# Kernel tuning notes

Measured on AMD Instinct MI355X. Metric: run time of the kernel, lower is better.

## Reference

```python
import jax, jax.numpy as jnp
import numpy as np
from jax import lax

WS = 7          # window size
SHIFT = 3       # shift size
HEADS = 16
DIM = 512
NREF = 100
H_IMG = 112
W_IMG = 112
BATCH = 2
HD = DIM // HEADS
SCALE = HD ** (-0.5)
EPS = 1e-5


def _layernorm(x, w, b):
    mu = jnp.mean(x, axis=-1, keepdims=True)
    var = jnp.mean((x - mu) ** 2, axis=-1, keepdims=True)
    return (x - mu) / jnp.sqrt(var + EPS) * w + b


def _rel_pos_index():
    coords = np.stack(np.meshgrid(np.arange(WS), np.arange(WS), indexing='ij'))  # (2,ws,ws)
    cf = coords.reshape(2, -1)
    rel = cf[:, :, None] - cf[:, None, :]
    rel = rel.transpose(1, 2, 0).astype(np.int64)
    rel[..., 0] += WS - 1
    rel[..., 1] += WS - 1
    rel[..., 0] *= 2 * WS - 1
    return rel.sum(-1).reshape(-1)  # (N*N,)

_RPI = _rel_pos_index()


def setup_inputs() -> dict:
    key = jax.random.key(0)
    ks = jax.random.split(key, 16)
    C = DIM
    s = 0.02
    x = jax.random.normal(ks[0], (BATCH, H_IMG * W_IMG, C), jnp.float32)
    x_ref = jax.random.normal(ks[1], (BATCH, NREF, C), jnp.float32)
    # shifted-window attention mask (standard Swin construction)
    img = np.zeros((H_IMG, W_IMG))
    cnt = 0
    for hs in (slice(0, -WS), slice(-WS, -SHIFT), slice(-SHIFT, None)):
        for ws_ in (slice(0, -WS), slice(-WS, -SHIFT), slice(-SHIFT, None)):
            img[hs, ws_] = cnt
            cnt += 1
    mw = img.reshape(H_IMG // WS, WS, W_IMG // WS, WS).transpose(0, 2, 1, 3).reshape(-1, WS * WS)
    am = mw[:, None, :] - mw[:, :, None]
    mask = jnp.asarray(np.where(am != 0, -100.0, 0.0), jnp.float32)  # (nW, N, N)
    return dict(
        x=x, x_ref=x_ref, mask=mask,
        norm1_w=jnp.ones((C,), jnp.float32), norm1_b=jnp.zeros((C,), jnp.float32),
        qkv_w=jax.random.normal(ks[2], (3 * C, C), jnp.float32) * s,
        qkv_b=jnp.zeros((3 * C,), jnp.float32),
        diff_mu=jax.random.normal(ks[3], (1, 1, C), jnp.float32),
        diff_logsigma=jax.random.normal(ks[4], (1, 1, C), jnp.float32) * s,
        rpb_table=jax.random.normal(ks[5], ((2 * WS - 1) ** 2, HEADS), jnp.float32) * s,
        ref_qk_w=jax.random.normal(ks[6], (2 * C, C), jnp.float32) * s,
        ref_qk_b=jnp.zeros((2 * C,), jnp.float32),
        conv_w=jax.random.normal(ks[7], (HEADS, HEADS, 3, 3), jnp.float32) * s,
        conv_b=jnp.zeros((HEADS,), jnp.float32),
        proj_w=jax.random.normal(ks[8], (C, C), jnp.float32) * s,
        proj_b=jnp.zeros((C,), jnp.float32),
        norm2_w=jnp.ones((C,), jnp.float32), norm2_b=jnp.zeros((C,), jnp.float32),
        fc1_w=jax.random.normal(ks[9], (4 * C, C), jnp.float32) * s,
        fc1_b=jnp.zeros((4 * C,), jnp.float32),
        fc2_w=jax.random.normal(ks[10], (C, 4 * C), jnp.float32) * s,
        fc2_b=jnp.zeros((C,), jnp.float32),
        Hh=H_IMG, Ww=W_IMG,
    )


def _window_attention(xw, mask, x_ref, qkv_w, qkv_b, diff_mu, diff_logsigma,
                      rpb_table, ref_qk_w, ref_qk_b, conv_w, conv_b, proj_w, proj_b):
    B_, N, C = xw.shape
    rB = x_ref.shape[0]
    n_win = B_ // rB
    qkv = (xw @ qkv_w.T + qkv_b).reshape(B_, N, 3, HEADS, HD).transpose(2, 0, 3, 1, 4)
    q, k, v = qkv[0], qkv[1], qkv[2]  # (B_, heads, N, hd)
    # reference tokens -> q/v with reparameterized shift/scale
    ref_qk = (x_ref @ ref_qk_w.T + ref_qk_b).reshape(rB, NREF, 2, C).transpose(2, 0, 1, 3)
    ref_q = diff_mu + jnp.exp(diff_logsigma) * ref_qk[0]
    ref_q = ref_q.reshape(rB, NREF, HEADS, HD).transpose(0, 2, 1, 3)
    ref_v = ref_qk[1].reshape(rB, NREF, HEADS, HD).transpose(0, 2, 1, 3)
    ref_k = jnp.repeat(ref_q, n_win, axis=0)  # (B_, heads, nref, hd)
    ref_v = jnp.repeat(ref_v, n_win, axis=0)
    ra = jnp.einsum('bhnd,bhrd->bhnr', q, ref_k)  # (B_, heads, N, nref)
    ra = ra.reshape(rB, n_win, HEADS, N, NREF).transpose(0, 2, 1, 3, 4).reshape(rB, HEADS, n_win * N, NREF)
    # 3 rounds of conv diffusion + layernorm(no affine) + gelu, residual
    for _ in range(3):
        u = lax.conv_general_dilated(ra, conv_w, (1, 1), 'SAME',
                                     dimension_numbers=('NCHW', 'OIHW', 'NCHW'))
        u = u + conv_b[None, :, None, None]
        mu = jnp.mean(u, axis=(-2, -1), keepdims=True)
        var = jnp.mean((u - mu) ** 2, axis=(-2, -1), keepdims=True)
        u = jax.nn.gelu((u - mu) / jnp.sqrt(var + EPS), approximate=False)
        ra = ra + u
    ra = ra.reshape(rB, HEADS, n_win, N, NREF).transpose(0, 2, 1, 3, 4).reshape(B_, HEADS, N, NREF)
    ra = jax.nn.softmax(ra, axis=-1)
    q_new = jnp.einsum('bhnr,bhrd->bhnd', ra, ref_v) * SCALE
    attn = jnp.einsum('bhnd,bhmd->bhnm', q_new, k)
    rpb = rpb_table[_RPI].reshape(N, N, HEADS).transpose(2, 0, 1)  # (heads, N, N)
    attn = attn + rpb[None]
    nW = mask.shape[0]
    attn = attn.reshape(B_ // nW, nW, HEADS, N, N) + mask[None, :, None]
    attn = jax.nn.softmax(attn.reshape(B_, HEADS, N, N), axis=-1)
    out = jnp.einsum('bhnm,bhmd->bhnd', attn, v).transpose(0, 2, 1, 3).reshape(B_, N, C)
    return out @ proj_w.T + proj_b


def reference(x, x_ref, mask, norm1_w, norm1_b, qkv_w, qkv_b, diff_mu, diff_logsigma,
              rpb_table, ref_qk_w, ref_qk_b, conv_w, conv_b, proj_w, proj_b,
              norm2_w, norm2_b, fc1_w, fc1_b, fc2_w, fc2_b, Hh, Ww):
    B, L, C = x.shape
    shortcut = x
    xn = _layernorm(x, norm1_w, norm1_b).reshape(B, Hh, Ww, C)
    # cyclic shift
    sx = jnp.roll(xn, (-SHIFT, -SHIFT), axis=(1, 2))
    # window partition -> (B*nWin, ws*ws, C)
    xw = sx.reshape(B, Hh // WS, WS, Ww // WS, WS, C).transpose(0, 1, 3, 2, 4, 5).reshape(-1, WS * WS, C)
    aw = _window_attention(xw, mask, x_ref, qkv_w, qkv_b, diff_mu, diff_logsigma,
                           rpb_table, ref_qk_w, ref_qk_b, conv_w, conv_b, proj_w, proj_b)
    # window reverse
    sx = aw.reshape(B, Hh // WS, Ww // WS, WS, WS, C).transpose(0, 1, 3, 2, 4, 5).reshape(B, Hh, Ww, C)
    xn = jnp.roll(sx, (SHIFT, SHIFT), axis=(1, 2)).reshape(B, L, C)
    x = shortcut + xn
    h = _layernorm(x, norm2_w, norm2_b)
    h = jax.nn.gelu(h @ fc1_w.T + fc1_b, approximate=False)
    return x + (h @ fc2_w.T + fc2_b)
```

## Files before the change

### kernel.cpp

```cpp
#include <hip/hip_runtime.h>
#include <hip/hip_bf16.h>

typedef __attribute__((ext_vector_type(8))) short short8;
typedef __attribute__((ext_vector_type(8))) unsigned short ushort8;
typedef __attribute__((ext_vector_type(4))) float f32x4;
typedef __attribute__((ext_vector_type(4))) unsigned int u32x4;
typedef __attribute__((ext_vector_type(2))) unsigned int u32x2;

#define DEV __device__ __forceinline__

DEV float gelu_f(float x) { return 0.5f * x * (1.f + erff(x * 0.70710678118654752440f)); }

DEV float bf2f(unsigned short s) {
  unsigned int t = ((unsigned int)s) << 16;
  float f; __builtin_memcpy(&f, &t, 4); return f;
}
DEV unsigned short f2bf(float f) {
  __hip_bfloat16 b = __float2bfloat16(f);
  unsigned short s; __builtin_memcpy(&s, &b, 2); return s;
}

DEV void async_copy16(void* lds, const void* g) {
  __builtin_amdgcn_global_load_lds(
      (const __attribute__((address_space(1))) unsigned int*)g,
      (__attribute__((address_space(3))) unsigned int*)lds, 16, 0, 0);
}

DEV void block_reduce2(float& s, float& s2) {
  __shared__ float red[8];
  int tid = threadIdx.x;
#pragma unroll
  for (int o = 32; o > 0; o >>= 1) { s += __shfl_down(s, o); s2 += __shfl_down(s2, o); }
  if ((tid & 63) == 0) { red[tid >> 6] = s; red[4 + (tid >> 6)] = s2; }
  __syncthreads();
  s  = red[0] + red[1] + red[2] + red[3];
  s2 = red[4] + red[5] + red[6] + red[7];
}

__global__ __launch_bounds__(256) void f2b_all_kernel(
    const float* __restrict__ qkv_w, const float* __restrict__ proj_w,
    const float* __restrict__ fc1_w, const float* __restrict__ fc2_w,
    __hip_bfloat16* __restrict__ wq, __hip_bfloat16* __restrict__ wp,
    __hip_bfloat16* __restrict__ w1, __hip_bfloat16* __restrict__ w2) {
  int i = blockIdx.x * 256 + threadIdx.x;
  const float* src; unsigned short* dst; int o;
  if (i < 98304)       { src = qkv_w;  dst = (unsigned short*)wq; o = i; }
  else if (i < 131072) { src = proj_w; dst = (unsigned short*)wp; o = i - 98304; }
  else if (i < 262144) { src = fc1_w;  dst = (unsigned short*)w1; o = i - 131072; }
  else                 { src = fc2_w;  dst = (unsigned short*)w2; o = i - 262144; }
  f32x4 a = *reinterpret_cast<const f32x4*>(&src[(size_t)o * 8]);
  f32x4 b = *reinterpret_cast<const f32x4*>(&src[(size_t)o * 8 + 4]);
  ushort8 v;
#pragma unroll
  for (int j = 0; j < 4; j++) { v[j] = f2bf(a[j]); v[4 + j] = f2bf(b[j]); }
  *reinterpret_cast<ushort8*>(&dst[(size_t)o * 8]) = v;
}

__global__ __launch_bounds__(256) void maskb_kernel(const float* __restrict__ mask,
                                                    unsigned short* __restrict__ maskB) {
  int i = blockIdx.x * 256 + threadIdx.x;
  int m = i % 56, rest = i / 56;
  int n = rest % 49, win = rest / 49;
  unsigned short v = 0;
  if (m < 49) v = f2bf(mask[((size_t)win * 49 + n) * 49 + m]);
  maskB[i] = v;
}

__global__ __launch_bounds__(256) void rpbt_kernel(const float* __restrict__ rpb,
                                                   unsigned short* __restrict__ rpbT) {
  int i = blockIdx.x * 256 + threadIdx.x;
  if (i >= 43904) return;
  int m = i % 56, rest = i / 56;
  int n = rest % 49, h = rest / 49;
  unsigned short v = 0;
  if (m < 49) {
    int rp = (n / 7 - m / 7 + 6) * 13 + (n % 7 - m % 7 + 6);
    v = f2bf(rpb[rp * 16 + h]);
  }
  rpbT[i] = v;
}

__global__ __launch_bounds__(256) void cwt_kernel(const float* __restrict__ cw,
                                                  unsigned short* __restrict__ cwT) {
  int i = blockIdx.x * 256 + threadIdx.x;
  if (i >= 2560) return;
  int co = i / 160, k = i % 160;
  unsigned short v = 0;
  if (k < 144) {
    int ci = k & 15, p = k >> 4;
    v = f2bf(cw[(co * 16 + ci) * 9 + p]);
  }
  cwT[i] = v;
}

__global__ __launch_bounds__(256) void ln1_window_kernel(
    const float* __restrict__ x, const float* __restrict__ w, const float* __restrict__ b,
    __hip_bfloat16* __restrict__ xw) {
  int tid = threadIdx.x;
  int wave = tid >> 6, lane = tid & 63;
  int t = blockIdx.x * 4 + wave;
  int b_ = t / 49, n = t % 49;
  int bb = b_ >> 8, win = b_ & 255;
  int wi = win >> 4, wj = win & 15;
  int ii = n / 7, jj = n % 7;
  int sh = (wi * 7 + ii + 3) % 112;
  int sw = (wj * 7 + jj + 3) % 112;
  const float* row = x + ((size_t)bb * 12544 + sh * 112 + sw) * 512;
  f32x4 v0 = *reinterpret_cast<const f32x4*>(&row[lane * 8]);
  f32x4 v1 = *reinterpret_cast<const f32x4*>(&row[lane * 8 + 4]);
  float s = 0.f, s2 = 0.f;
#pragma unroll
  for (int j = 0; j < 4; j++) {
    s += v0[j] + v1[j];
    s2 += v0[j] * v0[j] + v1[j] * v1[j];
  }
#pragma unroll
  for (int o = 1; o < 64; o <<= 1) { s += __shfl_xor(s, o); s2 += __shfl_xor(s2, o); }
  float mu = s * (1.f / 512.f);
  float rstd = rsqrtf(s2 * (1.f / 512.f) - mu * mu + 1e-5f);
  f32x4 w0 = *reinterpret_cast<const f32x4*>(&w[lane * 8]);
  f32x4 w1 = *reinterpret_cast<const f32x4*>(&w[lane * 8 + 4]);
  f32x4 c0 = *reinterpret_cast<const f32x4*>(&b[lane * 8]);
  f32x4 c1 = *reinterpret_cast<const f32x4*>(&b[lane * 8 + 4]);
  ushort8 o8;
#pragma unroll
  for (int j = 0; j < 4; j++) {
    o8[j]     = f2bf((v0[j] - mu) * rstd * w0[j] + c0[j]);
    o8[4 + j] = f2bf((v1[j] - mu) * rstd * w1[j] + c1[j]);
  }
  *reinterpret_cast<ushort8*>((unsigned short*)xw + (size_t)t * 512 + lane * 8) = o8;
}

template <int EPI>
__global__ __launch_bounds__(256) void gemm_bt(
    const __hip_bfloat16* __restrict__ A, const __hip_bfloat16* __restrict__ B,
    const float* __restrict__ bias, float* __restrict__ outF,
    __hip_bfloat16* __restrict__ outB, int M, int N, int K) {
  __shared__ __align__(16) __hip_bfloat16 As[2][128 * 64];
  __shared__ __align__(16) __hip_bfloat16 Bs[2][128 * 64];
  int nn = N >> 7;
  int nblk = gridDim.x;
  int bid = blockIdx.x;
  int xcd = bid & 7, slot = bid >> 3;
  int q8 = nblk >> 3, r8 = nblk & 7;
  int base = xcd < r8 ? xcd * (q8 + 1) : r8 * (q8 + 1) + (xcd - r8) * q8;
  int lin = base + slot;
  int m0 = (lin / nn) << 7, n0 = (lin % nn) << 7;
  int tid = threadIdx.x;
  int wave = tid >> 6, lane = tid & 63;
  int wm = (wave & 1) * 64, wn = (wave >> 1) * 64;
  int lrow = lane & 15, kq = lane >> 4;
  int srow = lane >> 3, scol = (lane & 7) * 8;
  int rb = wave * 32;
  const __hip_bfloat16* Abase = A + (size_t)m0 * K;
  const __hip_bfloat16* Bbase = B + (size_t)n0 * K;
#pragma unroll
  for (int i = 0; i < 4; i++) {
    int row = rb + i * 8 + srow;
    async_copy16(&As[0][(rb + i * 8) * 64], &Abase[(size_t)row * K + scol]);
    async_copy16(&Bs[0][(rb + i * 8) * 64], &Bbase[(size_t)row * K + scol]);
  }
  __syncthreads();
  f32x4 acc[4][4] = {};
  int nk = K >> 6;
  for (int t = 0; t < nk; t++) {
    int cur = t & 1;
    if (t + 1 < nk) {
      int k0 = (t + 1) << 6;
#pragma unroll
      for (int i = 0; i < 4; i++) {
        int row = rb + i * 8 + srow;
        async_copy16(&As[cur ^ 1][(rb + i * 8) * 64], &Abase[(size_t)row * K + k0 + scol]);
        async_copy16(&Bs[cur ^ 1][(rb + i * 8) * 64], &Bbase[(size_t)row * K + k0 + scol]);
      }
    }
#pragma unroll
    for (int ks = 0; ks < 2; ks++) {
      short8 af[4], bf[4];
#pragma unroll
      for (int u = 0; u < 4; u++) {
        af[u] = *reinterpret_cast<const short8*>(&As[cur][(wm + u * 16 + lrow) * 64 + ks * 32 + kq * 8]);
        bf[u] = *reinterpret_cast<const short8*>(&Bs[cur][(wn + u * 16 + lrow) * 64 + ks * 32 + kq * 8]);
      }
#pragma unroll
      for (int tm = 0; tm < 4; tm++)
#pragma unroll
        for (int tn = 0; tn < 4; tn++)
          acc[tm][tn] = __builtin_amdgcn_mfma_f32_16x16x32_bf16(af[tm], bf[tn], acc[tm][tn], 0, 0, 0);
    }
    __syncthreads();
  }
#pragma unroll
  for (int tm = 0; tm < 4; tm++) {
#pragma unroll
    for (int tn = 0; tn < 4; tn++) {
      int col = n0 + wn + tn * 16 + lrow;
      float bv = bias[col];
#pragma unroll
      for (int r = 0; r < 4; r++) {
        int row = m0 + wm + tm * 16 + kq * 4 + r;
        float v = acc[tm][tn][r] + bv;
        if (EPI == 4) {
          if (col < 512)
            ((unsigned short*)outB)[(size_t)row * 512 + col] = f2bf(v);
          else
            ((unsigned short*)outF)[(size_t)row * 1024 + (col - 512)] = f2bf(v);
        } else {
          size_t o = (size_t)row * N + col;
          if (EPI == 1) outB[o] = __float2bfloat16(v);
          else if (EPI == 2) outB[o] = __float2bfloat16(gelu_f(v));
          else outF[o] += v;
        }
      }
    }
  }
}

__global__ __launch_bounds__(256) void ref_kernel(
    const float* __restrict__ x_ref, const float* __restrict__ w, const float* __restrict__ bias,
    const float* __restrict__ diff_mu, const float* __restrict__ diff_ls,
    unsigned short* __restrict__ refq, unsigned short* __restrict__ refvT) {
  int blk = blockIdx.x;
  int b = blk / 100, r = blk % 100;
  __shared__ float xs[512];
  int tid = threadIdx.x;
  const float* xr = x_ref + (size_t)(b * 100 + r) * 512;
  xs[tid] = xr[tid];
  xs[tid + 256] = xr[tid + 256];
  __syncthreads();
#pragma unroll
  for (int cc = 0; cc < 4; cc++) {
    int c = cc * 256 + tid;
    const float* wr = w + (size_t)c * 512;
    float s = bias[c];
    for (int k = 0; k < 512; k++) s += xs[k] * wr[k];
    if (c < 512) {
      float v = diff_mu[c] + expf(diff_ls[c]) * s;
      int hh = c >> 5, d = c & 31;
      refq[((size_t)(b * 16 + hh) * 100 + r) * 32 + d] = f2bf(v);
    } else {
      int c2 = c - 512, hh = c2 >> 5, d = c2 & 31;
      refvT[(((size_t)b * 16 + hh) * 32 + d) * 128 + r] = f2bf(s);
    }
  }
  if (r < 28) {
#pragma unroll
    for (int j = 0; j < 2; j++) {
      int idx = j * 256 + tid;
      int hh = idx >> 5, d = idx & 31;
      refvT[(((size_t)b * 16 + hh) * 32 + d) * 128 + 100 + r] = 0;
    }
  }
}

__global__ __launch_bounds__(256) void ra_kernel(
    const __hip_bfloat16* __restrict__ q, const unsigned short* __restrict__ refq,
    __hip_bfloat16* __restrict__ ra) {
  __shared__ __align__(16) unsigned short q_s[64 * 40];
  __shared__ __align__(16) unsigned short rq_s[112 * 40];
  int bid = blockIdx.x;
  int blk = (bid & 7) * 1024 + (bid >> 3);
  int b_ = blk >> 4, h = blk & 15;
  int rb = b_ >> 8, win = b_ & 255;
  int tid = threadIdx.x;
  int wave = tid >> 6, lane = tid & 63;
  int lrow = lane & 15, kq = lane >> 4;
  u32x4 z4 = {};
  const unsigned short* qb = (const unsigned short*)q + (size_t)b_ * 49 * 512 + h * 32;
  for (int i = tid; i < 196; i += 256) {
    int n = i >> 2, c = i & 3;
    *reinterpret_cast<u32x4*>(&q_s[n * 40 + c * 8]) =
        *reinterpret_cast<const u32x4*>(&qb[n * 512 + c * 8]);
  }
  for (int i = tid; i < 60; i += 256) {
    int n = 49 + (i >> 2), c = i & 3;
    *reinterpret_cast<u32x4*>(&q_s[n * 40 + c * 8]) = z4;
  }
  const unsigned short* rqg = refq + (size_t)(rb * 16 + h) * 3200;
  for (int i = tid; i < 400; i += 256) {
    int r = i >> 2, c = i & 3;
    *reinterpret_cast<u32x4*>(&rq_s[r * 40 + c * 8]) =
        *reinterpret_cast<const u32x4*>(&rqg[r * 32 + c * 8]);
  }
  for (int i = tid; i < 48; i += 256) {
    int r = 100 + (i >> 2), c = i & 3;
    *reinterpret_cast<u32x4*>(&rq_s[r * 40 + c * 8]) = z4;
  }
  __syncthreads();
  short8 a = *reinterpret_cast<const short8*>(&q_s[(wave * 16 + lrow) * 40 + kq * 8]);
  unsigned short* ra_base = (unsigned short*)ra + ((size_t)(rb * 16 + h) * 12544 + win * 49) * 100;
  f32x4 zero = {};
#pragma unroll
  for (int nt = 0; nt < 7; nt++) {
    short8 b = *reinterpret_cast<const short8*>(&rq_s[(nt * 16 + lrow) * 40 + kq * 8]);
    f32x4 c = __builtin_amdgcn_mfma_f32_16x16x32_bf16(a, b, zero, 0, 0, 0);
    int col = nt * 16 + lrow;
#pragma unroll
    for (int r = 0; r < 4; r++) {
      int n = wave * 16 + kq * 4 + r;
      if (n < 49 && col < 100) ra_base[n * 100 + col] = f2bf(c[r]);
    }
  }
}

DEV int swzi(int pl, int ci) {
  int byte = (pl << 5) + (ci << 1);
  byte ^= ((pl >> 2) & 3) << 4;
  return byte >> 1;
}
__global__ __launch_bounds__(256, 6) void conv_kernel(
    const __hip_bfloat16* __restrict__ ra_, const unsigned short* __restrict__ cwT,
    const float* __restrict__ cb,
    __hip_bfloat16* __restrict__ u_, float* __restrict__ psum, float* __restrict__ psumsq) {
  __shared__ __align__(16) unsigned short in_s[6 * 103 * 16];
  __shared__ __align__(16) unsigned short st_s[4 * 16 * 36];
  __shared__ float sred_s[4][16], sred_s2[4][16];
  const unsigned short* ra = (const unsigned short*)ra_;
  unsigned short* u = (unsigned short*)u_;
  int ytb = blockIdx.x;
  int yt = (ytb & 7) * 392 + (ytb >> 3);
  int bb = blockIdx.y;
  int y0 = yt * 4;
  int tid = threadIdx.x;
  int wave = tid >> 6, lane = tid & 63;
  int lrow = lane & 15, kq = lane >> 4;
  for (int i = tid; i < 288; i += 256) {
    int ci = i & 15, rem = i >> 4;
    int yl = rem / 3, xs = rem % 3;
    int xl = (xs == 0) ? 0 : (100 + xs);
    in_s[swzi(yl * 103 + xl, ci)] = 0;
  }
  if (tid < 192) {
    int unit = tid >> 1, par = tid & 1;
    int ci = unit / 6, yl = unit % 6;
    int gy = y0 - 1 + yl;
    bool rv = (gy >= 0 && gy < 12544);
    const unsigned short* rp = ra + (((size_t)bb * 16 + ci) * 12544 + (rv ? gy : 0)) * 100;
    int plb = yl * 103 + 1;
#pragma unroll 4
    for (int c = par; c < 25; c += 2) {
      u32x2 d = {0u, 0u};
      if (rv) d = *reinterpret_cast<const u32x2*>(&rp[c * 4]);
      int pl = plb + c * 4;
      in_s[swzi(pl + 0, ci)] = (unsigned short)(d[0] & 0xffff);
      in_s[swzi(pl + 1, ci)] = (unsigned short)(d[0] >> 16);
      in_s[swzi(pl + 2, ci)] = (unsigned short)(d[1] & 0xffff);
      in_s[swzi(pl + 3, ci)] = (unsigned short)(d[1] >> 16);
    }
  }
  __syncthreads();

  short8 afr[5];
#pragma unroll
  for (int c = 0; c < 5; c++)
    afr[c] = *reinterpret_cast<const short8*>(&cwT[lrow * 160 + c * 32 + kq * 8]);
  int kqh = kq >> 1, ci0 = (kq & 1) * 8;
  int kyA[5], kxA[5];
#pragma unroll
  for (int c = 0; c < 5; c++) {
    int p = c * 2 + kqh; if (p > 8) p = 0;
    kyA[c] = p / 3; kxA[c] = p % 3;
  }
  float bias_r[4];
#pragma unroll
  for (int r = 0; r < 4; r++) bias_r[r] = cb[kq * 4 + r];
  float s_r[4] = {0.f, 0.f, 0.f, 0.f}, s2_r[4] = {0.f, 0.f, 0.f, 0.f};

  int yl = wave;
  int gy = y0 + yl;
  unsigned short* stw = &st_s[wave * 16 * 36];
  int seg = lane >> 2, part = lane & 3;
  const size_t ubase = ((size_t)bb * 16 * 12544 + gy) * 100;
#pragma unroll
  for (int xp = 0; xp < 4; xp++) {
#pragma unroll
    for (int xh = 0; xh < 2; xh++) {
      int xg = xp * 2 + xh;
      if (xg >= 7) break;
      int px = xg * 16 + lrow;
      int pxc = px < 100 ? px : 99;
      f32x4 acc = {};
#pragma unroll
      for (int c = 0; c < 5; c++) {
        short8 bfrag = *reinterpret_cast<const short8*>(
            &in_s[swzi((yl + kyA[c]) * 103 + pxc + kxA[c], ci0)]);
        acc = __builtin_amdgcn_mfma_f32_16x16x32_bf16(afr[c], bfrag, acc, 0, 0, 0);
      }
      bool valid = px < 100;
#pragma unroll
      for (int r = 0; r < 4; r++) {
        float v = acc[r] + bias_r[r];
        if (valid) {
          stw[(kq * 4 + r) * 36 + xh * 16 + lrow] = f2bf(v);
          s_r[r] += v; s2_r[r] += v * v;
        }
      }
    }
    unsigned short* ug = u + ubase + (size_t)seg * 1254400;
    if (xp < 3) {
      u32x2 d0 = *reinterpret_cast<const u32x2*>(&stw[seg * 36 + part * 4]);
      u32x2 d1 = *reinterpret_cast<const u32x2*>(&stw[seg * 36 + 16 + part * 4]);
      *reinterpret_cast<u32x2*>(&ug[xp * 32 + part * 4]) = d0;
      *reinterpret_cast<u32x2*>(&ug[xp * 32 + 16 + part * 4]) = d1;
    } else if (lane < 16) {
      u32x2 d = *reinterpret_cast<const u32x2*>(&st_s[wave * 16 * 36 + lane * 36]);
      *reinterpret_cast<u32x2*>(&u[ubase + (size_t)lane * 1254400 + 96]) = d;
    }
  }
#pragma unroll
  for (int o = 1; o < 16; o <<= 1)
#pragma unroll
    for (int r = 0; r < 4; r++) { s_r[r] += __shfl_xor(s_r[r], o); s2_r[r] += __shfl_xor(s2_r[r], o); }
  if (lrow == 0)
#pragma unroll
    for (int r = 0; r < 4; r++) { sred_s[wave][kq * 4 + r] = s_r[r]; sred_s2[wave][kq * 4 + r] = s2_r[r]; }
  __syncthreads();
  if (tid < 16) {
    float s  = sred_s[0][tid] + sred_s[1][tid] + sred_s[2][tid] + sred_s[3][tid];
    float s2 = sred_s2[0][tid] + sred_s2[1][tid] + sred_s2[2][tid] + sred_s2[3][tid];
    size_t pi = ((size_t)bb * 3136 + yt) * 16 + tid;
    psum[pi] = s; psumsq[pi] = s2;
  }
}

__global__ __launch_bounds__(256) void conv_stats_kernel(
    const float* __restrict__ psum, const float* __restrict__ psumsq, float* __restrict__ stats) {
  int g = blockIdx.x;
  int bb = g >> 4, co = g & 15;
  int tid = threadIdx.x;
  float s = 0.f, s2 = 0.f;
  for (int t = tid; t < 3136; t += 256) {
    size_t pi = ((size_t)bb * 3136 + t) * 16 + co;
    s += psum[pi];
    s2 += psumsq[pi];
  }
  block_reduce2(s, s2);
  if (tid == 0) {
    const float inv = 1.f / 1254400.f;
    float mu = s * inv;
    float var = s2 * inv - mu * mu;
    stats[g * 2] = mu;
    stats[g * 2 + 1] = rsqrtf(var + 1e-5f);
  }
}

__global__ __launch_bounds__(256) void conv_apply_kernel(
    __hip_bfloat16* __restrict__ ra, const __hip_bfloat16* __restrict__ u,
    const float* __restrict__ stats) {
  const int total8 = 5017600;
  int stride = gridDim.x * 256;
  for (int i = blockIdx.x * 256 + threadIdx.x; i < total8; i += stride) {
    int g = i / 156800;
    float mu = stats[g * 2], rstd = stats[g * 2 + 1];
    ushort8 uu = reinterpret_cast<const ushort8*>(u)[i];
    ushort8 rr = reinterpret_cast<const ushort8*>(ra)[i];
    ushort8 oo;
#pragma unroll
    for (int j = 0; j < 8; j++) {
      float rv = bf2f(rr[j]) + gelu_f((bf2f(uu[j]) - mu) * rstd);
      oo[j] = f2bf(rv);
    }
    reinterpret_cast<ushort8*>(ra)[i] = oo;
  }
}

template <int FUSE>
__global__ __launch_bounds__(256, 8) void attn_kernel(
    const __hip_bfloat16* __restrict__ ra_, const __hip_bfloat16* __restrict__ u_,
    const float* __restrict__ stats, const unsigned short* __restrict__ refvT,
    const __hip_bfloat16* __restrict__ kv_, const unsigned short* __restrict__ rpbT,
    const unsigned short* __restrict__ maskB, __hip_bfloat16* __restrict__ att_) {
  __shared__ __align__(16) char smem[18944];
  unsigned short* P1 = (unsigned short*)smem;
  unsigned short* P2 = (unsigned short*)smem;
  unsigned short* vT = (unsigned short*)(smem + 9216);
  unsigned short* qn = (unsigned short*)(smem + 13824);

#define LSUM(n) (*reinterpret_cast<float*>(&qn[(n) * 40 + 32]))

  int bid = blockIdx.x;
  int blk = (bid & 7) * 1024 + (bid >> 3);
  int b_ = blk >> 4, h = blk & 15;
  int rb = b_ >> 8, win = b_ & 255;
  int tid = threadIdx.x;
  int wave = tid >> 6, lane = tid & 63;
  int lrow = lane & 15, kq = lane >> 4;
  const unsigned short* ra = (const unsigned short*)ra_;
  const unsigned short* ug = (const unsigned short*)u_;
  const unsigned short* kv = (const unsigned short*)kv_;
  unsigned short* att = (unsigned short*)att_;
  u32x2 zz = {};

  if (tid < 64) LSUM(tid) = 1.0f;
  float mu = 0.f, rstd = 0.f;
  if (FUSE) { mu = stats[(rb * 16 + h) * 2]; rstd = stats[(rb * 16 + h) * 2 + 1]; }

  const size_t tile_off = ((size_t)(rb * 16 + h) * 12544 + win * 49) * 100;
  const unsigned short* rab = ra + tile_off;
  const unsigned short* uab = ug + tile_off;
  for (int i = tid; i < 1225; i += 256) {
    int n = i / 25, c = i % 25;
    u32x2 rv = *reinterpret_cast<const u32x2*>(&rab[n * 100 + c * 4]);
    if (FUSE) {
      u32x2 uv = *reinterpret_cast<const u32x2*>(&uab[n * 100 + c * 4]);
      unsigned short rr4[4] = {(unsigned short)(rv[0] & 0xffff), (unsigned short)(rv[0] >> 16),
                               (unsigned short)(rv[1] & 0xffff), (unsigned short)(rv[1] >> 16)};
      unsigned short uu4[4] = {(unsigned short)(uv[0] & 0xffff), (unsigned short)(uv[0] >> 16),
                               (unsigned short)(uv[1] & 0xffff), (unsigned short)(uv[1] >> 16)};
      unsigned short o4[4];
#pragma unroll
      for (int j = 0; j < 4; j++)
        o4[j] = f2bf(bf2f(rr4[j]) + gelu_f((bf2f(uu4[j]) - mu) * rstd));
      u32x2 w;
      w[0] = (unsigned int)o4[0] | ((unsigned int)o4[1] << 16);
      w[1] = (unsigned int)o4[2] | ((unsigned int)o4[3] << 16);
      *reinterpret_cast<u32x2*>(&P1[n * 136 + c * 4]) = w;
    } else {
      *reinterpret_cast<u32x2*>(&P1[n * 136 + c * 4]) = rv;
    }
  }
  for (int i = tid; i < 343; i += 256) {
    int n = i / 7, c = i % 7;
    *reinterpret_cast<u32x2*>(&P1[n * 136 + 100 + c * 4]) = zz;
  }
  __syncthreads();

  if (tid < 196) {
    int n = tid >> 2, q = tid & 3;
    unsigned short* row = P1 + n * 136 + q * 25;
    float e[25];
#pragma unroll
    for (int r = 0; r < 25; r++) e[r] = bf2f(row[r]);
    float mx = -1e30f;
#pragma unroll
    for (int r = 0; r < 25; r++) mx = fmaxf(mx, e[r]);
    mx = fmaxf(mx, __shfl_xor(mx, 1));
    mx = fmaxf(mx, __shfl_xor(mx, 2));
    float sm = 0.f;
#pragma unroll
    for (int r = 0; r < 25; r++) { e[r] = __expf(e[r] - mx); sm += e[r]; }
    sm += __shfl_xor(sm, 1);
    sm += __shfl_xor(sm, 2);
#pragma unroll
    for (int r = 0; r < 25; r++) row[r] = f2bf(e[r]);
    if (q == 0) LSUM(n) = sm;
  }
  __syncthreads();

  const unsigned short* rvtg = refvT + (size_t)(rb * 16 + h) * 4096;
  f32x4 acc1[2] = {};
#pragma unroll
  for (int ks = 0; ks < 4; ks++) {
    short8 a = *reinterpret_cast<const short8*>(&P1[(wave * 16 + lrow) * 136 + ks * 32 + kq * 8]);
#pragma unroll
    for (int dt = 0; dt < 2; dt++) {
      short8 b = *reinterpret_cast<const short8*>(&rvtg[(dt * 16 + lrow) * 128 + ks * 32 + kq * 8]);
      acc1[dt] = __builtin_amdgcn_mfma_f32_16x16x32_bf16(a, b, acc1[dt], 0, 0, 0);
    }
  }
  float invl[4];
#pragma unroll
  for (int r = 0; r < 4; r++)
    invl[r] = 0.17677669529663688f / LSUM(wave * 16 + kq * 4 + r);
#pragma unroll
  for (int dt = 0; dt < 2; dt++)
#pragma unroll
    for (int r = 0; r < 4; r++) {
      int n = wave * 16 + kq * 4 + r;
      qn[n * 40 + dt * 16 + lrow] = f2bf(acc1[dt][r] * invl[r]);
    }
  __syncthreads();

  const unsigned short* kvb = kv + (size_t)b_ * 49 * 1024;
  for (int i = tid; i < 196; i += 256) {
    int m = i >> 2, dg = (i & 3) * 8;
    ushort8 vv = *reinterpret_cast<const ushort8*>(&kvb[m * 1024 + 512 + h * 32 + dg]);
#pragma unroll
    for (int j = 0; j < 8; j++) vT[(dg + j) * 72 + m] = vv[j];
  }
  for (int i = tid; i < 480; i += 256) vT[(i / 15) * 72 + 49 + i % 15] = 0;
  __syncthreads();

  const unsigned short* bt = maskB + (size_t)win * 2744;
  const unsigned short* rt = rpbT + (size_t)h * 2744;
  short8 aq = *reinterpret_cast<const short8*>(&qn[(wave * 16 + lrow) * 40 + kq * 8]);
  f32x4 zero = {};
  float val[4][4];
#pragma unroll
  for (int mt = 0; mt < 4; mt++) {
    int mrow = mt * 16 + lrow;
    int mc = mrow < 49 ? mrow : 48;
    short8 bk = *reinterpret_cast<const short8*>(&kvb[mc * 1024 + h * 32 + kq * 8]);
    f32x4 lg = __builtin_amdgcn_mfma_f32_16x16x32_bf16(aq, bk, zero, 0, 0, 0);
    int m = mrow;
#pragma unroll
    for (int r = 0; r < 4; r++) {
      int n = wave * 16 + kq * 4 + r;
      float v;
      if (m < 49 && n < 49)
        v = lg[r] + bf2f(rt[n * 56 + m]) + bf2f(bt[n * 56 + m]);
      else v = -1e30f;
      val[mt][r] = v;
    }
  }
#pragma unroll
  for (int r = 0; r < 4; r++) {
    float mx = -1e30f;
#pragma unroll
    for (int mt = 0; mt < 4; mt++) mx = fmaxf(mx, val[mt][r]);
    mx = fmaxf(mx, __shfl_xor(mx, 1)); mx = fmaxf(mx, __shfl_xor(mx, 2));
    mx = fmaxf(mx, __shfl_xor(mx, 4)); mx = fmaxf(mx, __shfl_xor(mx, 8));
    float sm = 0.f, e[4];
#pragma unroll
    for (int mt = 0; mt < 4; mt++) { e[mt] = __expf(val[mt][r] - mx); sm += e[mt]; }
    sm += __shfl_xor(sm, 1); sm += __shfl_xor(sm, 2);
    sm += __shfl_xor(sm, 4); sm += __shfl_xor(sm, 8);
    float inv = 1.f / sm;
    int n = wave * 16 + kq * 4 + r;
#pragma unroll
    for (int mt = 0; mt < 4; mt++) P2[n * 72 + mt * 16 + lrow] = f2bf(e[mt] * inv);
  }
  __syncthreads();

  f32x4 acc2[2] = {};
#pragma unroll
  for (int ks = 0; ks < 2; ks++) {
    short8 ap = *reinterpret_cast<const short8*>(&P2[(wave * 16 + lrow) * 72 + ks * 32 + kq * 8]);
#pragma unroll
    for (int dt = 0; dt < 2; dt++) {
      short8 bv = *reinterpret_cast<const short8*>(&vT[(dt * 16 + lrow) * 72 + ks * 32 + kq * 8]);
      acc2[dt] = __builtin_amdgcn_mfma_f32_16x16x32_bf16(ap, bv, acc2[dt], 0, 0, 0);
    }
  }
  unsigned short* ab = att + (size_t)b_ * 49 * 512 + h * 32;
#pragma unroll
  for (int dt = 0; dt < 2; dt++)
#pragma unroll
    for (int r = 0; r < 4; r++) {
      int n = wave * 16 + kq * 4 + r;
      if (n < 49) ab[n * 512 + dt * 16 + lrow] = f2bf(acc2[dt][r]);
    }
#undef LSUM
}

__global__ __launch_bounds__(256) void resid_ln2_kernel(
    const float* __restrict__ x, const __hip_bfloat16* __restrict__ proj_out,
    const float* __restrict__ w2, const float* __restrict__ b2,
    float* __restrict__ out, __hip_bfloat16* __restrict__ hout) {
  int tid = threadIdx.x;
  int wave = tid >> 6, lane = tid & 63;
  int blk = blockIdx.x * 4 + wave;
  int bb = blk / 12544, l = blk % 12544;
  int hh = l / 112, ww = l % 112;
  int hs = (hh + 109) % 112, wsx = (ww + 109) % 112;
  int t = (bb * 256 + (hs / 7) * 16 + (wsx / 7)) * 49 + (hs % 7) * 7 + (wsx % 7);
  const float* xr = x + (size_t)blk * 512 + lane * 8;
  const unsigned short* pr = (const unsigned short*)proj_out + (size_t)t * 512 + lane * 8;
  f32x4 x0 = *reinterpret_cast<const f32x4*>(xr);
  f32x4 x1 = *reinterpret_cast<const f32x4*>(xr + 4);
  ushort8 p8 = *reinterpret_cast<const ushort8*>(pr);
  float v[8];
#pragma unroll
  for (int j = 0; j < 4; j++) {
    v[j]     = x0[j] + bf2f(p8[j]);
    v[4 + j] = x1[j] + bf2f(p8[4 + j]);
  }
  float s = 0.f, s2 = 0.f;
#pragma unroll
  for (int j = 0; j < 8; j++) { s += v[j]; s2 += v[j] * v[j]; }
  float* orow = out + (size_t)blk * 512 + lane * 8;
  f32x4 o0, o1;
#pragma unroll
  for (int j = 0; j < 4; j++) { o0[j] = v[j]; o1[j] = v[4 + j]; }
  *reinterpret_cast<f32x4*>(orow) = o0;
  *reinterpret_cast<f32x4*>(orow + 4) = o1;
#pragma unroll
  for (int o = 1; o < 64; o <<= 1) { s += __shfl_xor(s, o); s2 += __shfl_xor(s2, o); }
  float mu = s * (1.f / 512.f);
  float rstd = rsqrtf(s2 * (1.f / 512.f) - mu * mu + 1e-5f);
  f32x4 w0 = *reinterpret_cast<const f32x4*>(&w2[lane * 8]);
  f32x4 w1 = *reinterpret_cast<const f32x4*>(&w2[lane * 8 + 4]);
  f32x4 c0 = *reinterpret_cast<const f32x4*>(&b2[lane * 8]);
  f32x4 c1 = *reinterpret_cast<const f32x4*>(&b2[lane * 8 + 4]);
  ushort8 h8;
#pragma unroll
  for (int j = 0; j < 4; j++) {
    h8[j]     = f2bf((v[j] - mu) * rstd * w0[j] + c0[j]);
    h8[4 + j] = f2bf((v[4 + j] - mu) * rstd * w1[j] + c1[j]);
  }
  *reinterpret_cast<ushort8*>((unsigned short*)hout + (size_t)blk * 512 + lane * 8) = h8;
}

extern "C" void kernel_launch(void* const* d_in, const int* in_sizes, int n_in,
                              void* d_out, int out_size, void* d_ws, size_t ws_size,
                              hipStream_t stream) {
  const float* x       = (const float*)d_in[0];
  const float* x_ref   = (const float*)d_in[1];
  const float* mask    = (const float*)d_in[2];
  const float* n1w     = (const float*)d_in[3];
  const float* n1b     = (const float*)d_in[4];
  const float* qkv_w   = (const float*)d_in[5];
  const float* qkv_b   = (const float*)d_in[6];
  const float* diff_mu = (const float*)d_in[7];
  const float* diff_ls = (const float*)d_in[8];
  const float* rpb     = (const float*)d_in[9];
  const float* ref_w   = (const float*)d_in[10];
  const float* ref_b   = (const float*)d_in[11];
  const float* conv_w  = (const float*)d_in[12];
  const float* conv_b  = (const float*)d_in[13];
  const float* proj_w  = (const float*)d_in[14];
  const float* proj_b  = (const float*)d_in[15];
  const float* n2w     = (const float*)d_in[16];
  const float* n2b     = (const float*)d_in[17];
  const float* fc1_w   = (const float*)d_in[18];
  const float* fc1_b   = (const float*)d_in[19];
  const float* fc2_w   = (const float*)d_in[20];
  const float* fc2_b   = (const float*)d_in[21];
  float* out = (float*)d_out;

  char* ws = (char*)d_ws;
  size_t off = 0;
  auto alloc = [&](size_t bytes) -> char* {
    char* p = ws + off;
    off += (bytes + 255) & ~(size_t)255;
    return p;
  };
  __hip_bfloat16* wq_bf = (__hip_bfloat16*)alloc(1536ULL * 512 * 2);
  __hip_bfloat16* wp_bf = (__hip_bfloat16*)alloc(512ULL * 512 * 2);
  __hip_bfloat16* w1_bf = (__hip_bfloat16*)alloc(2048ULL * 512 * 2);
  __hip_bfloat16* w2_bf = (__hip_bfloat16*)alloc(512ULL * 2048 * 2);
  unsigned short* refq  = (unsigned short*)alloc(2ULL * 16 * 100 * 32 * 2);
  unsigned short* refvT = (unsigned short*)alloc(2ULL * 16 * 32 * 128 * 2);
  unsigned short* maskB = (unsigned short*)alloc(256ULL * 49 * 56 * 2);
  unsigned short* rpbT  = (unsigned short*)alloc(16ULL * 49 * 56 * 2);
  unsigned short* cwT   = (unsigned short*)alloc(2560ULL * 2);
  float* psum  = (float*)alloc(2ULL * 3136 * 16 * 4);
  float* psumq = (float*)alloc(2ULL * 3136 * 16 * 4);
  float* stats = (float*)alloc(64 * 4);
  char* regX  = alloc(25088ULL * 512 * 2);
  char* regQ  = alloc(25088ULL * 512 * 2);
  char* regRA = alloc(2ULL * 16 * 12544 * 100 * 2);
  char* regU  = alloc(2ULL * 16 * 12544 * 100 * 2);

  __hip_bfloat16* xw_bf   = (__hip_bfloat16*)regX;
  __hip_bfloat16* att_bf  = (__hip_bfloat16*)regX;
  __hip_bfloat16* q_bf    = (__hip_bfloat16*)regQ;
  __hip_bfloat16* h_bf    = (__hip_bfloat16*)regQ;
  __hip_bfloat16* ra      = (__hip_bfloat16*)regRA;
  __hip_bfloat16* hg      = (__hip_bfloat16*)regRA;
  __hip_bfloat16* u       = (__hip_bfloat16*)regU;
  __hip_bfloat16* proj_bf = (__hip_bfloat16*)(regU + 51380224);

  const size_t kv_bytes = 25088ULL * 1024 * 2;
  bool fused = (ws_size >= off + kv_bytes);
  __hip_bfloat16* kv_bf = fused ? (__hip_bfloat16*)alloc(kv_bytes)
                                : (__hip_bfloat16*)regU;

  f2b_all_kernel<<<1536, 256, 0, stream>>>(qkv_w, proj_w, fc1_w, fc2_w,
                                           wq_bf, wp_bf, w1_bf, w2_bf);
  maskb_kernel<<<2744, 256, 0, stream>>>(mask, maskB);
  rpbt_kernel<<<172, 256, 0, stream>>>(rpb, rpbT);
  cwt_kernel<<<10, 256, 0, stream>>>(conv_w, cwT);
  ln1_window_kernel<<<6272, 256, 0, stream>>>(x, n1w, n1b, xw_bf);
  if (fused) {
    gemm_bt<4><<<2352, 256, 0, stream>>>(xw_bf, wq_bf, qkv_b, (float*)kv_bf, q_bf,
                                         25088, 1536, 512);
  } else {
    gemm_bt<1><<<784, 256, 0, stream>>>(xw_bf, wq_bf, qkv_b, nullptr, q_bf,
                                        25088, 512, 512);
  }
  ref_kernel<<<200, 256, 0, stream>>>(x_ref, ref_w, ref_b, diff_mu, diff_ls, refq, refvT);
  ra_kernel<<<8192, 256, 0, stream>>>(q_bf, refq, ra);
  for (int rd = 0; rd < 3; rd++) {
    conv_kernel<<<dim3(3136, 2), 256, 0, stream>>>(ra, cwT, conv_b, u, psum, psumq);
    conv_stats_kernel<<<32, 256, 0, stream>>>(psum, psumq, stats);
    if (rd < 2 || !fused)
      conv_apply_kernel<<<4096, 256, 0, stream>>>(ra, u, stats);
  }
  if (!fused)
    gemm_bt<1><<<1568, 256, 0, stream>>>(xw_bf, wq_bf + 512 * 512, qkv_b + 512,
                                         nullptr, kv_bf, 25088, 1024, 512);
  if (fused)
    attn_kernel<1><<<8192, 256, 0, stream>>>(ra, u, stats, refvT, kv_bf, rpbT, maskB, att_bf);
  else
    attn_kernel<0><<<8192, 256, 0, stream>>>(ra, u, stats, refvT, kv_bf, rpbT, maskB, att_bf);
  gemm_bt<1><<<784, 256, 0, stream>>>(att_bf, wp_bf, proj_b, nullptr, proj_bf,
                                      25088, 512, 512);
  resid_ln2_kernel<<<6272, 256, 0, stream>>>(x, proj_bf, n2w, n2b, out, h_bf);
  for (int ch = 0; ch < 2; ch++) {
    const __hip_bfloat16* hA = h_bf + (size_t)ch * 12544 * 512;
    gemm_bt<2><<<1568, 256, 0, stream>>>(hA, w1_bf, fc1_b, nullptr, hg,
                                         12544, 2048, 512);
    gemm_bt<3><<<392, 256, 0, stream>>>(hg, w2_bf, fc2_b,
                                        out + (size_t)ch * 12544 * 512, nullptr,
                                        12544, 512, 2048);
  }
}
```

Before: 1.087 ms.

## Shrink GEMM tile to 64x128 single-buffered LDS for higher occupancy

Result: faster. 1.008 ms (-7.2%).

```diff
diff --git a/kernel.cpp b/kernel.cpp
--- a/kernel.cpp
+++ b/kernel.cpp
@@ -132,12 +132,12 @@
 }
 
 template <int EPI>
-__global__ __launch_bounds__(256) void gemm_bt(
+__global__ __launch_bounds__(256, 6) void gemm_bt(
     const __hip_bfloat16* __restrict__ A, const __hip_bfloat16* __restrict__ B,
     const float* __restrict__ bias, float* __restrict__ outF,
     __hip_bfloat16* __restrict__ outB, int M, int N, int K) {
-  __shared__ __align__(16) __hip_bfloat16 As[2][128 * 64];
-  __shared__ __align__(16) __hip_bfloat16 Bs[2][128 * 64];
+  __shared__ __align__(16) __hip_bfloat16 As[64 * 64];
+  __shared__ __align__(16) __hip_bfloat16 Bs[128 * 64];
   int nn = N >> 7;
   int nblk = gridDim.x;
   int bid = blockIdx.x;
@@ -145,45 +145,38 @@
   int q8 = nblk >> 3, r8 = nblk & 7;
   int base = xcd < r8 ? xcd * (q8 + 1) : r8 * (q8 + 1) + (xcd - r8) * q8;
   int lin = base + slot;
-  int m0 = (lin / nn) << 7, n0 = (lin % nn) << 7;
+  int m0 = (lin / nn) << 6, n0 = (lin % nn) << 7;
   int tid = threadIdx.x;
   int wave = tid >> 6, lane = tid & 63;
-  int wm = (wave & 1) * 64, wn = (wave >> 1) * 64;
+  int wr = (wave >> 1) * 32, wc = (wave & 1) * 64;
   int lrow = lane & 15, kq = lane >> 4;
   int srow = lane >> 3, scol = (lane & 7) * 8;
-  int rb = wave * 32;
   const __hip_bfloat16* Abase = A + (size_t)m0 * K;
   const __hip_bfloat16* Bbase = B + (size_t)n0 * K;
-#pragma unroll
-  for (int i = 0; i < 4; i++) {
-    int row = rb + i * 8 + srow;
-    async_copy16(&As[0][(rb + i * 8) * 64], &Abase[(size_t)row * K + scol]);
-    async_copy16(&Bs[0][(rb + i * 8) * 64], &Bbase[(size_t)row * K + scol]);
-  }
-  __syncthreads();
-  f32x4 acc[4][4] = {};
-  int nk = K >> 6;
-  for (int t = 0; t < nk; t++) {
-    int cur = t & 1;
-    if (t + 1 < nk) {
-      int k0 = (t + 1) << 6;
-#pragma unroll
-      for (int i = 0; i < 4; i++) {
-        int row = rb + i * 8 + srow;
-        async_copy16(&As[cur ^ 1][(rb + i * 8) * 64], &Abase[(size_t)row * K + k0 + scol]);
-        async_copy16(&Bs[cur ^ 1][(rb + i * 8) * 64], &Bbase[(size_t)row * K + k0 + scol]);
-      }
-    }
+  f32x4 acc[2][4] = {};
+  for (int k0 = 0; k0 < K; k0 += 64) {
+#pragma unroll
+    for (int i = 0; i < 2; i++) {
+      int row = wave * 16 + i * 8;
+      async_copy16(&As[row * 64], &Abase[(size_t)(row + srow) * K + k0 + scol]);
+    }
+#pragma unroll
+    for (int i = 0; i < 4; i++) {
+      int row = wave * 32 + i * 8;
+      async_copy16(&Bs[row * 64], &Bbase[(size_t)(row + srow) * K + k0 + scol]);
+    }
+    __syncthreads();
 #pragma unroll
     for (int ks = 0; ks < 2; ks++) {
-      short8 af[4], bf[4];
-#pragma unroll
-      for (int u = 0; u < 4; u++) {
-        af[u] = *reinterpret_cast<const short8*>(&As[cur][(wm + u * 16 + lrow) * 64 + ks * 32 + kq * 8]);
-        bf[u] = *reinterpret_cast<const short8*>(&Bs[cur][(wn + u * 16 + lrow) * 64 + ks * 32 + kq * 8]);
-      }
-#pragma unroll
-      for (int tm = 0; tm < 4; tm++)
+      short8 af[2], bf[4];
+#pragma unroll
+      for (int t = 0; t < 2; t++)
+        af[t] = *reinterpret_cast<const short8*>(&As[(wr + t * 16 + lrow) * 64 + ks * 32 + kq * 8]);
+#pragma unroll
+      for (int t = 0; t < 4; t++)
+        bf[t] = *reinterpret_cast<const short8*>(&Bs[(wc + t * 16 + lrow) * 64 + ks * 32 + kq * 8]);
+#pragma unroll
+      for (int tm = 0; tm < 2; tm++)
 #pragma unroll
         for (int tn = 0; tn < 4; tn++)
           acc[tm][tn] = __builtin_amdgcn_mfma_f32_16x16x32_bf16(af[tm], bf[tn], acc[tm][tn], 0, 0, 0);
@@ -191,14 +184,14 @@
     __syncthreads();
   }
 #pragma unroll
-  for (int tm = 0; tm < 4; tm++) {
+  for (int tm = 0; tm < 2; tm++) {
 #pragma unroll
     for (int tn = 0; tn < 4; tn++) {
-      int col = n0 + wn + tn * 16 + lrow;
+      int col = n0 + wc + tn * 16 + lrow;
       float bv = bias[col];
 #pragma unroll
       for (int r = 0; r < 4; r++) {
-        int row = m0 + wm + tm * 16 + kq * 4 + r;
+        int row = m0 + wr + tm * 16 + kq * 4 + r;
         float v = acc[tm][tn][r] + bv;
         if (EPI == 4) {
           if (col < 512)
@@ -763,11 +756,11 @@
   cwt_kernel<<<10, 256, 0, stream>>>(conv_w, cwT);
   ln1_window_kernel<<<6272, 256, 0, stream>>>(x, n1w, n1b, xw_bf);
   if (fused) {
-    gemm_bt<4><<<2352, 256, 0, stream>>>(xw_bf, wq_bf, qkv_b, (float*)kv_bf, q_bf,
+    gemm_bt<4><<<4704, 256, 0, stream>>>(xw_bf, wq_bf, qkv_b, (float*)kv_bf, q_bf,
                                          25088, 1536, 512);
   } else {
-    gemm_bt<1><<<784, 256, 0, stream>>>(xw_bf, wq_bf, qkv_b, nullptr, q_bf,
-                                        25088, 512, 512);
+    gemm_bt<1><<<1568, 256, 0, stream>>>(xw_bf, wq_bf, qkv_b, nullptr, q_bf,
+                                         25088, 512, 512);
   }
   ref_kernel<<<200, 256, 0, stream>>>(x_ref, ref_w, ref_b, diff_mu, diff_ls, refq, refvT);
   ra_kernel<<<8192, 256, 0, stream>>>(q_bf, refq, ra);
@@ -778,20 +771,20 @@
       conv_apply_kernel<<<4096, 256, 0, stream>>>(ra, u, stats);
   }
   if (!fused)
-    gemm_bt<1><<<1568, 256, 0, stream>>>(xw_bf, wq_bf + 512 * 512, qkv_b + 512,
+    gemm_bt<1><<<3136, 256, 0, stream>>>(xw_bf, wq_bf + 512 * 512, qkv_b + 512,
                                          nullptr, kv_bf, 25088, 1024, 512);
   if (fused)
     attn_kernel<1><<<8192, 256, 0, stream>>>(ra, u, stats, refvT, kv_bf, rpbT, maskB, att_bf);
   else
     attn_kernel<0><<<8192, 256, 0, stream>>>(ra, u, stats, refvT, kv_bf, rpbT, maskB, att_bf);
-  gemm_bt<1><<<784, 256, 0, stream>>>(att_bf, wp_bf, proj_b, nullptr, proj_bf,
-                                      25088, 512, 512);
+  gemm_bt<1><<<1568, 256, 0, stream>>>(att_bf, wp_bf, proj_b, nullptr, proj_bf,
+                                       25088, 512, 512);
   resid_ln2_kernel<<<6272, 256, 0, stream>>>(x, proj_bf, n2w, n2b, out, h_bf);
   for (int ch = 0; ch < 2; ch++) {
     const __hip_bfloat16* hA = h_bf + (size_t)ch * 12544 * 512;
-    gemm_bt<2><<<1568, 256, 0, stream>>>(hA, w1_bf, fc1_b, nullptr, hg,
+    gemm_bt<2><<<3136, 256, 0, stream>>>(hA, w1_bf, fc1_b, nullptr, hg,
                                          12544, 2048, 512);
-    gemm_bt<3><<<392, 256, 0, stream>>>(hg, w2_bf, fc2_b,
+    gemm_bt<3><<<784, 256, 0, stream>>>(hg, w2_bf, fc2_b,
                                         out + (size_t)ch * 12544 * 512, nullptr,
                                         12544, 512, 2048);
   }
```
